# Performance work log

Hardware: AMD Instinct MI355X
Metric: run time of the kernel (lower is better)

Reference implementation:

```python
import jax, jax.numpy as jnp
import numpy as np

B, T, C = 256, 256, 147
BPM, H_DIM, NH = 32, 64, 4
HD = H_DIM // NH


def setup_inputs() -> dict:
    key = jax.random.key(0)
    ks = jax.random.split(key, 12)
    def lin(k, fan_in, fan_out):
        bound = 1.0 / np.sqrt(fan_in)
        kw, kb = jax.random.split(k)
        W = jax.random.uniform(kw, (fan_in, fan_out), jnp.float32, -bound, bound)
        b = jax.random.uniform(kb, (fan_out,), jnp.float32, -bound, bound)
        return W, b
    Wq, bq = lin(ks[0], C, H_DIM)
    Wk, bk = lin(ks[1], C, H_DIM)
    Wv, bv = lin(ks[2], C, H_DIM)
    Wb, bb = lin(ks[3], BPM, H_DIM)
    Wo, bo = lin(ks[4], H_DIM, C)
    pose = jax.random.normal(ks[5], (B, T, C), jnp.float32)
    bpm_emb = jax.random.normal(ks[6], (B, BPM), jnp.float32)
    return {"pose": pose, "bpm_emb": bpm_emb,
            "Wq": Wq, "bq": bq, "Wk": Wk, "bk": bk, "Wv": Wv, "bv": bv,
            "Wb": Wb, "bb": bb, "Wo": Wo, "bo": bo}


def reference(pose, bpm_emb, Wq, bq, Wk, bk, Wv, bv, Wb, bb, Wo, bo):
    Bb, Tt, Cc = pose.shape
    scale = HD ** -0.5
    # projections -> [B, H, T, hd]
    def split_heads(x):
        return x.reshape(Bb, Tt, NH, HD).transpose(0, 2, 1, 3)
    q = split_heads(pose @ Wq + bq)
    k = split_heads(pose @ Wk + bk)
    v = split_heads(pose @ Wv + bv)
    # bpm-conditioned key bias: [B, H, 1, hd]
    bpm_feat = (bpm_emb @ Wb + bb).reshape(Bb, 1, NH, HD).transpose(0, 2, 1, 3)
    k = k + bpm_feat
    # attention
    scores = jnp.einsum('bhqd,bhkd->bhqk', q, k) * scale
    attn = jax.nn.softmax(scores, axis=-1)
    out = jnp.einsum('bhqk,bhkd->bhqd', attn, v)
    out = out.transpose(0, 2, 1, 3).reshape(Bb, Tt, NH * HD)
    return out @ Wo + bo
```

## Files before the change

### kernel.cpp

```cpp
#include <hip/hip_runtime.h>

constexpr int kC = 147, kH = 64, kHD = 16, kBPM = 32;

typedef __attribute__((ext_vector_type(8)))  short bf16x8;
typedef __attribute__((ext_vector_type(4)))  float f32x4;
typedef __attribute__((ext_vector_type(16))) float f32x16;
typedef __attribute__((ext_vector_type(4)))  short s16x4;

__device__ __forceinline__ short f2bf(float f) {
    unsigned u = __builtin_bit_cast(unsigned, f);
    u += 0x7fffu + ((u >> 16) & 1u);
    return (short)(u >> 16);
}
#define MFMA16(a,b,c) __builtin_amdgcn_mfma_f32_16x16x32_bf16((a),(b),(c),0,0,0)
#define MFMA32(a,b,c) __builtin_amdgcn_mfma_f32_32x32x16_bf16((a),(b),(c),0,0,0)

constexpr int QS  = 72;
constexpr int VS  = 264;
constexpr int PS  = 40;
constexpr int WSS = 168;
constexpr int WOS = 72;

__global__ __launch_bounds__(512, 2) void fused_kernel(
    const float* __restrict__ pose, const float* __restrict__ bpm_emb,
    const float* __restrict__ Wq, const float* __restrict__ bq,
    const float* __restrict__ Wk, const float* __restrict__ bk,
    const float* __restrict__ Wv, const float* __restrict__ bv,
    const float* __restrict__ Wb, const float* __restrict__ bb,
    const float* __restrict__ Wo, const float* __restrict__ bo,
    float* __restrict__ out)
{
    __shared__ __align__(16) short qs[256 * QS];
    __shared__ __align__(16) short ks_[256 * QS];
    __shared__ __align__(16) short vt[kH * VS];
    __shared__ __align__(16) short Ws[11520];
    __shared__ __align__(16) short Pt[8 * 32 * PS];
    __shared__ float l_s[8 * 128];
    __shared__ float bias_s[192];

    const int tid = threadIdx.x;
    const int w = tid >> 6, lane = tid & 63;
    const int ll = lane & 15, lq = lane >> 4;
    const int lm = lane & 31, lh = lane >> 5;
    const int b = blockIdx.x;
    const size_t pbase = (size_t)b * 256 * kC;

    if (tid < 192) {
        const int m = tid >> 6, c = tid & 63;
        float a = ((m == 0) ? bq : (m == 1) ? bk : bv)[c];
        if (m == 1) {
            a += bb[c];
            #pragma unroll
            for (int k2 = 0; k2 < kBPM; ++k2)
                a = fmaf(bpm_emb[b * kBPM + k2], Wb[k2 * kH + c], a);
        }
        if (m == 0) a *= 0.25f;
        bias_s[tid] = a;
    }
    for (int i = tid; i < kH * 160; i += 512) {
        const int k = i >> 6, c = i & 63;
        Ws[c * WSS + k] = f2bf((k < kC) ? Wq[k * kH + c] * 0.25f : 0.f);
    }
    bf16x8 pf[2][5];
    #pragma unroll
    for (int nt = 0; nt < 2; ++nt) {
        const int row = w * 32 + nt * 16 + ll;
        const float* prow = pose + pbase + (size_t)row * kC;
        #pragma unroll
        for (int ksp = 0; ksp < 5; ++ksp) {
            const int c0 = ksp * 32 + lq * 8;
            float v[8];
            if (c0 + 8 <= kC) {
                const float4 f0 = *(const float4*)(prow + c0);
                const float4 f1 = *(const float4*)(prow + c0 + 4);
                v[0]=f0.x; v[1]=f0.y; v[2]=f0.z; v[3]=f0.w;
                v[4]=f1.x; v[5]=f1.y; v[6]=f1.z; v[7]=f1.w;
            } else {
                #pragma unroll
                for (int e = 0; e < 8; ++e) v[e] = (c0 + e < kC) ? prow[c0 + e] : 0.f;
            }
            bf16x8 t;
            #pragma unroll
            for (int e = 0; e < 8; ++e) t[e] = f2bf(v[e]);
            pf[nt][ksp] = t;
        }
    }
    __syncthreads();

    for (int m = 0; m < 3; ++m) {
        f32x4 acc[4][2];
        #pragma unroll
        for (int mt = 0; mt < 4; ++mt)
            #pragma unroll
            for (int nt = 0; nt < 2; ++nt) acc[mt][nt] = (f32x4){0.f,0.f,0.f,0.f};
        #pragma unroll
        for (int ksp = 0; ksp < 5; ++ksp)
            #pragma unroll
            for (int mt = 0; mt < 4; ++mt) {
                const bf16x8 wf = *(const bf16x8*)(Ws + (mt*16 + ll)*WSS + ksp*32 + lq*8);
                acc[mt][0] = MFMA16(wf, pf[0][ksp], acc[mt][0]);
                acc[mt][1] = MFMA16(wf, pf[1][ksp], acc[mt][1]);
            }
        __syncthreads();
        if (m == 0) {
            for (int i = tid; i < kH * 160; i += 512) {
                const int k = i >> 6, c = i & 63;
                Ws[c * WSS + k] = f2bf((k < kC) ? Wk[k * kH + c] : 0.f);
            }
        } else if (m == 1) {
            for (int i = tid; i < kH * 160; i += 512) {
                const int k = i >> 6, c = i & 63;
                Ws[c * WSS + k] = f2bf((k < kC) ? Wv[k * kH + c] : 0.f);
            }
        } else {
            for (int i = tid; i < 160 * kH; i += 512) {
                const int k = i / 160, n = i - k * 160;
                Ws[n * WOS + k] = f2bf((n < kC) ? Wo[k * kC + n] : 0.f);
            }
        }
        #pragma unroll
        for (int mt = 0; mt < 4; ++mt) {
            const int c0 = mt * 16 + 4 * lq;
            const float4 bv4 = *(const float4*)&bias_s[m * kH + c0];
            #pragma unroll
            for (int nt = 0; nt < 2; ++nt) {
                const int row = w * 32 + nt * 16 + ll;
                if (m < 2) {
                    s16x4 pk;
                    pk[0] = f2bf(acc[mt][nt][0] + bv4.x);
                    pk[1] = f2bf(acc[mt][nt][1] + bv4.y);
                    pk[2] = f2bf(acc[mt][nt][2] + bv4.z);
                    pk[3] = f2bf(acc[mt][nt][3] + bv4.w);
                    *(s16x4*)((m == 0 ? qs : ks_) + row * QS + c0) = pk;
                } else {
                    vt[(c0 + 0) * VS + row] = f2bf(acc[mt][nt][0] + bv4.x);
                    vt[(c0 + 1) * VS + row] = f2bf(acc[mt][nt][1] + bv4.y);
                    vt[(c0 + 2) * VS + row] = f2bf(acc[mt][nt][2] + bv4.z);
                    vt[(c0 + 3) * VS + row] = f2bf(acc[mt][nt][3] + bv4.w);
                }
            }
        }
        __syncthreads();
    }

    const int h = w >> 1;
    const int q0 = (w & 1) * 128;
    bf16x8 qf[4];
    #pragma unroll
    for (int s32 = 0; s32 < 4; ++s32)
        qf[s32] = *(const bf16x8*)(qs + (q0 + s32*32 + lm) * QS + h*16 + lh*8);

    f32x4 oacc[4][2];
    #pragma unroll
    for (int s32 = 0; s32 < 4; ++s32) {
        oacc[s32][0] = (f32x4){0.f,0.f,0.f,0.f};
        oacc[s32][1] = (f32x4){0.f,0.f,0.f,0.f};
    }
    float lp[4] = {0.f, 0.f, 0.f, 0.f};
    short* Pw = Pt + w * 32 * PS;

    for (int jb = 0; jb < 8; ++jb) {
        const int j0 = jb * 32;
        const bf16x8 kf = *(const bf16x8*)(ks_ + (j0 + lm) * QS + h*16 + lh*8);
        const bf16x8 vf = *(const bf16x8*)(vt + (h*16 + ll) * VS + j0 + lq*8);
        #pragma unroll
        for (int s32 = 0; s32 < 4; ++s32) {
            const f32x16 z16 = {0.f,0.f,0.f,0.f,0.f,0.f,0.f,0.f,
                                0.f,0.f,0.f,0.f,0.f,0.f,0.f,0.f};
            const f32x16 s = MFMA32(kf, qf[s32], z16);
            float sum = 0.f;
            #pragma unroll
            for (int g = 0; g < 4; ++g) {
                const float p0 = __expf(s[4*g + 0]);
                const float p1 = __expf(s[4*g + 1]);
                const float p2 = __expf(s[4*g + 2]);
                const float p3 = __expf(s[4*g + 3]);
                sum += (p0 + p1) + (p2 + p3);
                s16x4 pk; pk[0] = f2bf(p0); pk[1] = f2bf(p1);
                pk[2] = f2bf(p2); pk[3] = f2bf(p3);
                *(s16x4*)(Pw + lm * PS + 8*g + 4*lh) = pk;
            }
            lp[s32] += sum;
            #pragma unroll
            for (int half = 0; half < 2; ++half) {
                const bf16x8 pfr = *(const bf16x8*)(Pw + (half*16 + ll) * PS + lq*8);
                oacc[s32][half] = MFMA16(vf, pfr, oacc[s32][half]);
            }
        }
    }
    #pragma unroll
    for (int s32 = 0; s32 < 4; ++s32) {
        const float l2 = lp[s32] + __shfl_xor(lp[s32], 32);
        if (lane < 32) l_s[w * 128 + s32 * 32 + lm] = l2;
    }
    #pragma unroll
    for (int s32 = 0; s32 < 4; ++s32)
        #pragma unroll
        for (int half = 0; half < 2; ++half) {
            const int qi = s32 * 32 + half * 16 + ll;
            const float inv = 1.f / l_s[w * 128 + qi];
            s16x4 pk;
            #pragma unroll
            for (int r = 0; r < 4; ++r) pk[r] = f2bf(oacc[s32][half][r] * inv);
            *(s16x4*)(qs + (q0 + qi) * QS + h*16 + 4*lq) = pk;
        }
    __syncthreads();

    bf16x8 xf[2][2];
    #pragma unroll
    for (int nt = 0; nt < 2; ++nt)
        #pragma unroll
        for (int k2 = 0; k2 < 2; ++k2)
            xf[nt][k2] = *(const bf16x8*)(qs + (w*32 + nt*16 + ll) * QS + k2*32 + lq*8);

    f32x4 po[10][2];
    #pragma unroll
    for (int mt = 0; mt < 10; ++mt) {
        po[mt][0] = (f32x4){0.f,0.f,0.f,0.f};
        po[mt][1] = (f32x4){0.f,0.f,0.f,0.f};
    }
    #pragma unroll
    for (int k2 = 0; k2 < 2; ++k2)
        #pragma unroll
        for (int mt = 0; mt < 10; ++mt) {
            const bf16x8 wf = *(const bf16x8*)(Ws + (mt*16 + ll) * WOS + k2*32 + lq*8);
            po[mt][0] = MFMA16(wf, xf[0][k2], po[mt][0]);
            po[mt][1] = MFMA16(wf, xf[1][k2], po[mt][1]);
        }
    #pragma unroll
    for (int mt = 0; mt < 10; ++mt) {
        const int c0 = mt * 16 + 4 * lq;
        #pragma unroll
        for (int nt = 0; nt < 2; ++nt) {
            const int row = w * 32 + nt * 16 + ll;
            float* orow = out + ((size_t)b * 256 + row) * kC;
            if (mt < 9) {
                const float4 bv4 = *(const float4*)(bo + c0);
                float4 o;
                o.x = po[mt][nt][0] + bv4.x; o.y = po[mt][nt][1] + bv4.y;
                o.z = po[mt][nt][2] + bv4.z; o.w = po[mt][nt][3] + bv4.w;
                *(float4*)(orow + c0) = o;
            } else {
                #pragma unroll
                for (int r = 0; r < 4; ++r) {
                    const int c = c0 + r;
                    if (c < kC) orow[c] = po[mt][nt][r] + bo[c];
                }
            }
        }
    }
}

extern "C" void kernel_launch(void* const* d_in, const int* in_sizes, int n_in,
                              void* d_out, int out_size, void* d_ws, size_t ws_size,
                              hipStream_t stream) {
    const float* pose    = (const float*)d_in[0];
    const float* bpm_emb = (const float*)d_in[1];
    const float* Wq = (const float*)d_in[2];  const float* bq = (const float*)d_in[3];
    const float* Wk = (const float*)d_in[4];  const float* bk = (const float*)d_in[5];
    const float* Wv = (const float*)d_in[6];  const float* bv = (const float*)d_in[7];
    const float* Wb = (const float*)d_in[8];  const float* bb = (const float*)d_in[9];
    const float* Wo = (const float*)d_in[10]; const float* bo = (const float*)d_in[11];
    float* out = (float*)d_out;

    fused_kernel<<<256, 512, 0, stream>>>(
        pose, bpm_emb, Wq, bq, Wk, bk, Wv, bv, Wb, bb, Wo, bo, out);
}
```

Measured before the change: 152.3 us.

## Double threads per block to 1024, alias weight and P buffers, use exp2

```diff
diff --git a/kernel.cpp b/kernel.cpp
--- a/kernel.cpp
+++ b/kernel.cpp
@@ -15,13 +15,20 @@
 #define MFMA16(a,b,c) __builtin_amdgcn_mfma_f32_16x16x32_bf16((a),(b),(c),0,0,0)
 #define MFMA32(a,b,c) __builtin_amdgcn_mfma_f32_32x32x16_bf16((a),(b),(c),0,0,0)
 
+#if __has_builtin(__builtin_amdgcn_exp2f)
+  #define EXP2(x) __builtin_amdgcn_exp2f(x)
+#else
+  #define EXP2(x) __expf((x) * 0.6931471805599453f)
+#endif
+constexpr float kQScale = 0.25f * 1.4426950408889634f;
+
 constexpr int QS  = 72;
 constexpr int VS  = 264;
 constexpr int PS  = 40;
 constexpr int WSS = 168;
 constexpr int WOS = 72;
 
-__global__ __launch_bounds__(512, 2) void fused_kernel(
+__global__ __launch_bounds__(1024, 4) void fused_kernel(
     const float* __restrict__ pose, const float* __restrict__ bpm_emb,
     const float* __restrict__ Wq, const float* __restrict__ bq,
     const float* __restrict__ Wk, const float* __restrict__ bk,
@@ -33,10 +40,11 @@
     __shared__ __align__(16) short qs[256 * QS];
     __shared__ __align__(16) short ks_[256 * QS];
     __shared__ __align__(16) short vt[kH * VS];
-    __shared__ __align__(16) short Ws[11520];
-    __shared__ __align__(16) short Pt[8 * 32 * PS];
-    __shared__ float l_s[8 * 128];
+    __shared__ __align__(16) short WsPt[20480];
+    __shared__ float l_s[16 * 64];
     __shared__ float bias_s[192];
+    short* const Ws = WsPt;
+    short* const Pt = WsPt;
 
     const int tid = threadIdx.x;
     const int w = tid >> 6, lane = tid & 63;
@@ -54,17 +62,16 @@
             for (int k2 = 0; k2 < kBPM; ++k2)
                 a = fmaf(bpm_emb[b * kBPM + k2], Wb[k2 * kH + c], a);
         }
-        if (m == 0) a *= 0.25f;
+        if (m == 0) a *= kQScale;
         bias_s[tid] = a;
     }
-    for (int i = tid; i < kH * 160; i += 512) {
+    for (int i = tid; i < kH * 160; i += 1024) {
         const int k = i >> 6, c = i & 63;
-        Ws[c * WSS + k] = f2bf((k < kC) ? Wq[k * kH + c] * 0.25f : 0.f);
-    }
-    bf16x8 pf[2][5];
-    #pragma unroll
-    for (int nt = 0; nt < 2; ++nt) {
-        const int row = w * 32 + nt * 16 + ll;
+        Ws[c * WSS + k] = f2bf((k < kC) ? Wq[k * kH + c] * kQScale : 0.f);
+    }
+    bf16x8 pf[5];
+    {
+        const int row = w * 16 + ll;
         const float* prow = pose + pbase + (size_t)row * kC;
         #pragma unroll
         for (int ksp = 0; ksp < 5; ++ksp) {
@@ -82,81 +89,70 @@
             bf16x8 t;
             #pragma unroll
             for (int e = 0; e < 8; ++e) t[e] = f2bf(v[e]);
-            pf[nt][ksp] = t;
+            pf[ksp] = t;
         }
     }
     __syncthreads();
 
     for (int m = 0; m < 3; ++m) {
-        f32x4 acc[4][2];
-        #pragma unroll
-        for (int mt = 0; mt < 4; ++mt)
-            #pragma unroll
-            for (int nt = 0; nt < 2; ++nt) acc[mt][nt] = (f32x4){0.f,0.f,0.f,0.f};
+        f32x4 acc[4];
+        #pragma unroll
+        for (int mt = 0; mt < 4; ++mt) acc[mt] = (f32x4){0.f,0.f,0.f,0.f};
         #pragma unroll
         for (int ksp = 0; ksp < 5; ++ksp)
             #pragma unroll
             for (int mt = 0; mt < 4; ++mt) {
                 const bf16x8 wf = *(const bf16x8*)(Ws + (mt*16 + ll)*WSS + ksp*32 + lq*8);
-                acc[mt][0] = MFMA16(wf, pf[0][ksp], acc[mt][0]);
-                acc[mt][1] = MFMA16(wf, pf[1][ksp], acc[mt][1]);
+                acc[mt] = MFMA16(wf, pf[ksp], acc[mt]);
             }
         __syncthreads();
         if (m == 0) {
-            for (int i = tid; i < kH * 160; i += 512) {
+            for (int i = tid; i < kH * 160; i += 1024) {
                 const int k = i >> 6, c = i & 63;
                 Ws[c * WSS + k] = f2bf((k < kC) ? Wk[k * kH + c] : 0.f);
             }
         } else if (m == 1) {
-            for (int i = tid; i < kH * 160; i += 512) {
+            for (int i = tid; i < kH * 160; i += 1024) {
                 const int k = i >> 6, c = i & 63;
                 Ws[c * WSS + k] = f2bf((k < kC) ? Wv[k * kH + c] : 0.f);
             }
-        } else {
-            for (int i = tid; i < 160 * kH; i += 512) {
-                const int k = i / 160, n = i - k * 160;
-                Ws[n * WOS + k] = f2bf((n < kC) ? Wo[k * kC + n] : 0.f);
-            }
-        }
+        }
+        const int row = w * 16 + ll;
         #pragma unroll
         for (int mt = 0; mt < 4; ++mt) {
             const int c0 = mt * 16 + 4 * lq;
             const float4 bv4 = *(const float4*)&bias_s[m * kH + c0];
-            #pragma unroll
-            for (int nt = 0; nt < 2; ++nt) {
-                const int row = w * 32 + nt * 16 + ll;
-                if (m < 2) {
-                    s16x4 pk;
-                    pk[0] = f2bf(acc[mt][nt][0] + bv4.x);
-                    pk[1] = f2bf(acc[mt][nt][1] + bv4.y);
-                    pk[2] = f2bf(acc[mt][nt][2] + bv4.z);
-                    pk[3] = f2bf(acc[mt][nt][3] + bv4.w);
-                    *(s16x4*)((m == 0 ? qs : ks_) + row * QS + c0) = pk;
-                } else {
-                    vt[(c0 + 0) * VS + row] = f2bf(acc[mt][nt][0] + bv4.x);
-                    vt[(c0 + 1) * VS + row] = f2bf(acc[mt][nt][1] + bv4.y);
-                    vt[(c0 + 2) * VS + row] = f2bf(acc[mt][nt][2] + bv4.z);
-                    vt[(c0 + 3) * VS + row] = f2bf(acc[mt][nt][3] + bv4.w);
-                }
+            if (m < 2) {
+                s16x4 pk;
+                pk[0] = f2bf(acc[mt][0] + bv4.x);
+                pk[1] = f2bf(acc[mt][1] + bv4.y);
+                pk[2] = f2bf(acc[mt][2] + bv4.z);
+                pk[3] = f2bf(acc[mt][3] + bv4.w);
+                *(s16x4*)((m == 0 ? qs : ks_) + row * QS + c0) = pk;
+            } else {
+                vt[(c0 + 0) * VS + row] = f2bf(acc[mt][0] + bv4.x);
+                vt[(c0 + 1) * VS + row] = f2bf(acc[mt][1] + bv4.y);
+                vt[(c0 + 2) * VS + row] = f2bf(acc[mt][2] + bv4.z);
+                vt[(c0 + 3) * VS + row] = f2bf(acc[mt][3] + bv4.w);
             }
         }
         __syncthreads();
     }
 
-    const int h = w >> 1;
-    const int q0 = (w & 1) * 128;
-    bf16x8 qf[4];
-    #pragma unroll
-    for (int s32 = 0; s32 < 4; ++s32)
+    const int h = w & 3;
+    const int q0 = (w >> 2) * 64;
+    bf16x8 qf[2];
+    #pragma unroll
+    for (int s32 = 0; s32 < 2; ++s32)
         qf[s32] = *(const bf16x8*)(qs + (q0 + s32*32 + lm) * QS + h*16 + lh*8);
 
-    f32x4 oacc[4][2];
-    #pragma unroll
-    for (int s32 = 0; s32 < 4; ++s32) {
+    f32x4 oacc[2][2];
+    #pragma unroll
+    for (int s32 = 0; s32 < 2; ++s32) {
         oacc[s32][0] = (f32x4){0.f,0.f,0.f,0.f};
         oacc[s32][1] = (f32x4){0.f,0.f,0.f,0.f};
     }
-    float lp[4] = {0.f, 0.f, 0.f, 0.f};
+    float lp[2] = {0.f, 0.f};
     short* Pw = Pt + w * 32 * PS;
 
     for (int jb = 0; jb < 8; ++jb) {
@@ -164,17 +160,17 @@
         const bf16x8 kf = *(const bf16x8*)(ks_ + (j0 + lm) * QS + h*16 + lh*8);
         const bf16x8 vf = *(const bf16x8*)(vt + (h*16 + ll) * VS + j0 + lq*8);
         #pragma unroll
-        for (int s32 = 0; s32 < 4; ++s32) {
+        for (int s32 = 0; s32 < 2; ++s32) {
             const f32x16 z16 = {0.f,0.f,0.f,0.f,0.f,0.f,0.f,0.f,
                                 0.f,0.f,0.f,0.f,0.f,0.f,0.f,0.f};
             const f32x16 s = MFMA32(kf, qf[s32], z16);
             float sum = 0.f;
             #pragma unroll
             for (int g = 0; g < 4; ++g) {
-                const float p0 = __expf(s[4*g + 0]);
-                const float p1 = __expf(s[4*g + 1]);
-                const float p2 = __expf(s[4*g + 2]);
-                const float p3 = __expf(s[4*g + 3]);
+                const float p0 = EXP2(s[4*g + 0]);
+                const float p1 = EXP2(s[4*g + 1]);
+                const float p2 = EXP2(s[4*g + 2]);
+                const float p3 = EXP2(s[4*g + 3]);
                 sum += (p0 + p1) + (p2 + p3);
                 s16x4 pk; pk[0] = f2bf(p0); pk[1] = f2bf(p1);
                 pk[2] = f2bf(p2); pk[3] = f2bf(p3);
@@ -189,16 +185,16 @@
         }
     }
     #pragma unroll
-    for (int s32 = 0; s32 < 4; ++s32) {
+    for (int s32 = 0; s32 < 2; ++s32) {
         const float l2 = lp[s32] + __shfl_xor(lp[s32], 32);
-        if (lane < 32) l_s[w * 128 + s32 * 32 + lm] = l2;
-    }
-    #pragma unroll
-    for (int s32 = 0; s32 < 4; ++s32)
+        if (lane < 32) l_s[w * 64 + s32 * 32 + lm] = l2;
+    }
+    #pragma unroll
+    for (int s32 = 0; s32 < 2; ++s32)
         #pragma unroll
         for (int half = 0; half < 2; ++half) {
             const int qi = s32 * 32 + half * 16 + ll;
-            const float inv = 1.f / l_s[w * 128 + qi];
+            const float inv = 1.f / l_s[w * 64 + qi];
             s16x4 pk;
             #pragma unroll
             for (int r = 0; r < 4; ++r) pk[r] = f2bf(oacc[s32][half][r] * inv);
@@ -206,45 +202,44 @@
         }
     __syncthreads();
 
-    bf16x8 xf[2][2];
-    #pragma unroll
-    for (int nt = 0; nt < 2; ++nt)
-        #pragma unroll
-        for (int k2 = 0; k2 < 2; ++k2)
-            xf[nt][k2] = *(const bf16x8*)(qs + (w*32 + nt*16 + ll) * QS + k2*32 + lq*8);
-
-    f32x4 po[10][2];
-    #pragma unroll
-    for (int mt = 0; mt < 10; ++mt) {
-        po[mt][0] = (f32x4){0.f,0.f,0.f,0.f};
-        po[mt][1] = (f32x4){0.f,0.f,0.f,0.f};
-    }
+    for (int i = tid; i < 160 * kH; i += 1024) {
+        const int k = i / 160, n = i - k * 160;
+        Ws[n * WOS + k] = f2bf((n < kC) ? Wo[k * kC + n] : 0.f);
+    }
+    __syncthreads();
+
+    bf16x8 xf[2];
+    #pragma unroll
+    for (int k2 = 0; k2 < 2; ++k2)
+        xf[k2] = *(const bf16x8*)(qs + (w*16 + ll) * QS + k2*32 + lq*8);
+
+    f32x4 po[10];
+    #pragma unroll
+    for (int mt = 0; mt < 10; ++mt) po[mt] = (f32x4){0.f,0.f,0.f,0.f};
     #pragma unroll
     for (int k2 = 0; k2 < 2; ++k2)
         #pragma unroll
         for (int mt = 0; mt < 10; ++mt) {
             const bf16x8 wf = *(const bf16x8*)(Ws + (mt*16 + ll) * WOS + k2*32 + lq*8);
-            po[mt][0] = MFMA16(wf, xf[0][k2], po[mt][0]);
-            po[mt][1] = MFMA16(wf, xf[1][k2], po[mt][1]);
-        }
-    #pragma unroll
-    for (int mt = 0; mt < 10; ++mt) {
-        const int c0 = mt * 16 + 4 * lq;
-        #pragma unroll
-        for (int nt = 0; nt < 2; ++nt) {
-            const int row = w * 32 + nt * 16 + ll;
-            float* orow = out + ((size_t)b * 256 + row) * kC;
+            po[mt] = MFMA16(wf, xf[k2], po[mt]);
+        }
+    {
+        const int row = w * 16 + ll;
+        float* orow = out + ((size_t)b * 256 + row) * kC;
+        #pragma unroll
+        for (int mt = 0; mt < 10; ++mt) {
+            const int c0 = mt * 16 + 4 * lq;
             if (mt < 9) {
                 const float4 bv4 = *(const float4*)(bo + c0);
                 float4 o;
-                o.x = po[mt][nt][0] + bv4.x; o.y = po[mt][nt][1] + bv4.y;
-                o.z = po[mt][nt][2] + bv4.z; o.w = po[mt][nt][3] + bv4.w;
+                o.x = po[mt][0] + bv4.x; o.y = po[mt][1] + bv4.y;
+                o.z = po[mt][2] + bv4.z; o.w = po[mt][3] + bv4.w;
                 *(float4*)(orow + c0) = o;
             } else {
                 #pragma unroll
                 for (int r = 0; r < 4; ++r) {
                     const int c = c0 + r;
-                    if (c < kC) orow[c] = po[mt][nt][r] + bo[c];
+                    if (c < kC) orow[c] = po[mt][r] + bo[c];
                 }
             }
         }
@@ -263,6 +258,6 @@
     const float* Wo = (const float*)d_in[10]; const float* bo = (const float*)d_in[11];
     float* out = (float*)d_out;
 
-    fused_kernel<<<256, 512, 0, stream>>>(
+    fused_kernel<<<256, 1024, 0, stream>>>(
         pose, bpm_emb, Wq, bq, Wk, bk, Wv, bv, Wb, bb, Wo, bo, out);
 }
```

Measured after the change: 138.3 us. -9.2%, faster.
